# Performance work log

Hardware: AMD Instinct MI355X
Metric: run time of the kernel (lower is better)

Reference implementation:

```python
import jax, jax.numpy as jnp
import numpy as np

B, L = 128, 4096
H, RH, D, K = 128, 64, 64, 512  # num_hiddens, residual_hiddens, embedding_dim, num_embeddings
BETA = 0.25  # commitment_cost


def conv1d(x, w, b=None, stride=1, pad=0):
    # x: (N, C, W); w: (O, I, K) torch layout
    y = jax.lax.conv_general_dilated(x, w, (stride,), [(pad, pad)],
                                     dimension_numbers=('NCW', 'OIW', 'NCW'))
    return y if b is None else y + b[None, :, None]


def convT1d(x, w, b=None, stride=2, pad=1):
    # torch ConvTranspose1d weight layout (in, out, k)
    k = w.shape[-1]
    w_t = jnp.flip(w, -1).transpose(1, 0, 2)  # (out, in, k)
    y = jax.lax.conv_general_dilated(x, w_t, (1,), [(k - 1 - pad, k - 1 - pad)],
                                     lhs_dilation=(stride,),
                                     dimension_numbers=('NCW', 'OIW', 'NCW'))
    return y if b is None else y + b[None, :, None]


def res_stack(x, layers):
    for w1, w2 in layers:
        h = conv1d(jax.nn.relu(x), w1, None, 1, 1)
        h = conv1d(jax.nn.relu(h), w2, None, 1, 0)
        x = x + h
    return jax.nn.relu(x)


def _forward(x, enc_w1, enc_b1, enc_w2, enc_b2, enc_w3, enc_b3,
             enc_r1a, enc_r1b, enc_r2a, enc_r2b, pre_vq_w, pre_vq_b, codebook,
             dec_w1, dec_b1, dec_r1a, dec_r1b, dec_r2a, dec_r2b,
             dec_ct1_w, dec_ct1_b, dec_ct2_w, dec_ct2_b):
    # ---- Encoder (compression_factor == 4) ----
    h = x[:, None, :]                                   # (B, 1, L)
    h = jax.nn.relu(conv1d(h, enc_w1, enc_b1, 2, 1))    # (B, H/2, L/2)
    h = jax.nn.relu(conv1d(h, enc_w2, enc_b2, 2, 1))    # (B, H, L/4)
    h = conv1d(h, enc_w3, enc_b3, 1, 1)
    h = res_stack(h, [(enc_r1a, enc_r1b), (enc_r2a, enc_r2b)])
    z = conv1d(h, pre_vq_w, pre_vq_b, 1, 0)             # (B, D, T)

    # ---- Vector quantization ----
    zt = z.transpose(0, 2, 1)                           # (B, T, D)
    flat = zt.reshape(-1, D)                            # (BT, D)
    dists = (jnp.sum(flat * flat, 1, keepdims=True)
             - 2.0 * flat @ codebook.T
             + jnp.sum(codebook * codebook, 1))         # (BT, K)
    idx = jnp.argmin(dists, axis=1)                     # (BT,)
    q = codebook[idx].reshape(zt.shape)                 # (B, T, D)

    e_latent = jnp.mean((jax.lax.stop_gradient(q) - zt) ** 2)
    q_latent = jnp.mean((q - jax.lax.stop_gradient(zt)) ** 2)
    loss = q_latent + BETA * e_latent
    q_st = zt + jax.lax.stop_gradient(q - zt)           # straight-through

    counts = jnp.zeros((K,), flat.dtype).at[idx].add(1.0)
    probs = counts / idx.shape[0]
    perplexity = jnp.exp(-jnp.sum(probs * jnp.log(probs + 1e-10)))

    # ---- Decoder (compression_factor == 4) ----
    hd = q_st.transpose(0, 2, 1)                        # (B, D, T)
    hd = conv1d(hd, dec_w1, dec_b1, 1, 1)               # (B, H, T)
    hd = res_stack(hd, [(dec_r1a, dec_r1b), (dec_r2a, dec_r2b)])
    hd = jax.nn.relu(convT1d(hd, dec_ct1_w, dec_ct1_b)) # (B, H/2, 2T)
    hd = convT1d(hd, dec_ct2_w, dec_ct2_b)              # (B, 1, 4T)
    recon = jnp.squeeze(hd)                             # (B, L)
    return loss, recon, perplexity


def setup_inputs() -> dict:
    key = jax.random.key(0)
    ks = jax.random.split(key, 32)
    n = lambda i, shape, s=0.05: jax.random.normal(ks[i], shape, jnp.float32) * s
    inp = {
        'x': jax.random.normal(ks[0], (B, L), jnp.float32),
        'enc_w1': n(1, (H // 2, 1, 4)), 'enc_b1': jnp.zeros((H // 2,), jnp.float32),
        'enc_w2': n(2, (H, H // 2, 4)), 'enc_b2': jnp.zeros((H,), jnp.float32),
        'enc_w3': n(3, (H, H, 3)), 'enc_b3': jnp.zeros((H,), jnp.float32),
        'enc_r1a': n(4, (RH, H, 3)), 'enc_r1b': n(5, (H, RH, 1)),
        'enc_r2a': n(6, (RH, H, 3)), 'enc_r2b': n(7, (H, RH, 1)),
        'pre_vq_w': n(8, (D, H, 1)), 'pre_vq_b': jnp.zeros((D,), jnp.float32),
        'codebook': jax.random.uniform(ks[9], (K, D), jnp.float32, -1.0 / K, 1.0 / K),
        'dec_w1': n(10, (H, D, 3)), 'dec_b1': jnp.zeros((H,), jnp.float32),
        'dec_r1a': n(11, (RH, H, 3)), 'dec_r1b': n(12, (H, RH, 1)),
        'dec_r2a': n(13, (RH, H, 3)), 'dec_r2b': n(14, (H, RH, 1)),
        'dec_ct1_w': n(15, (H, H // 2, 4)), 'dec_ct1_b': jnp.zeros((H // 2,), jnp.float32),
        'dec_ct2_w': n(16, (H // 2, 1, 4)), 'dec_ct2_b': jnp.zeros((1,), jnp.float32),
    }
    return inp


def reference(x, enc_w1, enc_b1, enc_w2, enc_b2, enc_w3, enc_b3,
              enc_r1a, enc_r1b, enc_r2a, enc_r2b, pre_vq_w, pre_vq_b, codebook,
              dec_w1, dec_b1, dec_r1a, dec_r1b, dec_r2a, dec_r2b,
              dec_ct1_w, dec_ct1_b, dec_ct2_w, dec_ct2_b):
    return _forward(x, enc_w1, enc_b1, enc_w2, enc_b2, enc_w3, enc_b3,
                    enc_r1a, enc_r1b, enc_r2a, enc_r2b, pre_vq_w, pre_vq_b, codebook,
                    dec_w1, dec_b1, dec_r1a, dec_r1b, dec_r2a, dec_r2b,
                    dec_ct1_w, dec_ct1_b, dec_ct2_w, dec_ct2_b)
```

## Files before the change

kernel.cpp:

```cpp
#include <hip/hip_runtime.h>
#include <hip/hip_bf16.h>
#include <math.h>

using bf16 = __hip_bfloat16;
typedef __attribute__((ext_vector_type(4))) float f32x4;
typedef __attribute__((ext_vector_type(8))) short s16x8;

#define MFMA16(a,b,c) __builtin_amdgcn_mfma_f32_16x16x32_bf16((a),(b),(c),0,0,0)


__device__ inline float bf2f(unsigned short u) {
    union { float f; unsigned v; } c; c.v = ((unsigned)u) << 16; return c.f;
}
__device__ inline unsigned short bfbits(float f) {
    union { bf16 h; unsigned short u; } c; c.h = __float2bfloat16(f); return c.u;
}
__device__ inline s16x8 relu8(s16x8 v) {
#pragma unroll
    for (int j = 0; j < 8; ++j)
        v[j] = (short)(((unsigned short)v[j] & 0x8000u) ? 0 : (unsigned short)v[j]);
    return v;
}

__global__ __launch_bounds__(256, 3) void encmid_k(
    const bf16* __restrict__ in, const bf16* __restrict__ w3t,
    const float* __restrict__ b3, const bf16* __restrict__ r1w1,
    const bf16* __restrict__ r1w2, const bf16* __restrict__ r2w1,
    const bf16* __restrict__ r2w2, bf16* __restrict__ out)
{
    __shared__ __align__(16) char smem[47872];
    char* sY = smem;
    char* sX = smem + 21760;
    char* sH = smem + 21760;
    const int tid = threadIdx.x;
    const int b   = blockIdx.y;
    const int l0  = blockIdx.x * 64;
    const bf16* inb = in + (size_t)b * 1024 * 128;

    for (int i = tid; i < 96 * 16; i += 256) {
        int t = i >> 4, c0 = (i & 15) * 8;
        int g = l0 - 16 + t;
        s16x8 v = {};
        if (g >= 0 && g < 1024) v = *(const s16x8*)(inb + (size_t)g * 128 + c0);
        *(s16x8*)(sX + ((t * 136 + c0) << 1)) = v;
    }
    __syncthreads();

    const int lane = tid & 63;
    const int wid  = __builtin_amdgcn_readfirstlane(tid >> 6);
    const int lr   = lane & 15;
    const int kg   = lane >> 4;
    const f32x4 zf4 = {0.f, 0.f, 0.f, 0.f};

    {
        const int co0 = wid * 32;
        f32x4 acc[2][5];
#pragma unroll
        for (int cf = 0; cf < 2; ++cf)
#pragma unroll
            for (int lf = 0; lf < 5; ++lf) acc[cf][lf] = zf4;
#pragma unroll
        for (int k = 0; k < 3; ++k) {
            const bf16* Ab = w3t + (size_t)k * 128 * 128;
#pragma unroll
            for (int ks = 0; ks < 4; ++ks) {
                s16x8 af[2];
#pragma unroll
                for (int cf = 0; cf < 2; ++cf)
                    af[cf] = *(const s16x8*)(Ab + (co0 + cf * 16 + lr) * 128 + ks * 32 + kg * 8);
                s16x8 bfr[5];
#pragma unroll
                for (int lf = 0; lf < 5; ++lf) {
                    int tx = lf * 16 + lr + 7 + k;
                    bfr[lf] = *(const s16x8*)(sX + ((tx * 136 + ks * 32 + kg * 8) << 1));
                }
#pragma unroll
                for (int cf = 0; cf < 2; ++cf)
#pragma unroll
                    for (int lf = 0; lf < 5; ++lf)
                        acc[cf][lf] = MFMA16(af[cf], bfr[lf], acc[cf][lf]);
            }
        }
        __syncthreads();
#pragma unroll
        for (int cf = 0; cf < 2; ++cf)
#pragma unroll
            for (int lf = 0; lf < 5; ++lf) {
                int row = lf * 16 + lr;
                int p   = l0 - 8 + row;
                int cb0 = co0 + cf * 16 + kg * 4;
                bool ok = (p >= 0 && p < 1024);
                float r[4];
#pragma unroll
                for (int j = 0; j < 4; ++j)
                    r[j] = ok ? (acc[cf][lf][j] + b3[cb0 + j]) : 0.f;
                uint2 pk;
                pk.x = (unsigned)bfbits(r[0]) | ((unsigned)bfbits(r[1]) << 16);
                pk.y = (unsigned)bfbits(r[2]) | ((unsigned)bfbits(r[3]) << 16);
                *(uint2*)(sY + ((row * 136 + cb0) << 1)) = pk;
            }
    }
    __syncthreads();

#pragma unroll 1
    for (int blk = 0; blk < 2; ++blk) {
        const bf16* w1 = blk ? r2w1 : r1w1;
        {
            const int co0 = wid * 16;
            f32x4 acc[5];
#pragma unroll
            for (int lf = 0; lf < 5; ++lf) acc[lf] = zf4;
#pragma unroll
            for (int k = 0; k < 3; ++k) {
                const bf16* Ab = w1 + (size_t)k * 64 * 128;
#pragma unroll
                for (int ks = 0; ks < 4; ++ks) {
                    s16x8 a = *(const s16x8*)(Ab + (co0 + lr) * 128 + ks * 32 + kg * 8);
                    s16x8 bfr[5];
#pragma unroll
                    for (int lf = 0; lf < 5; ++lf) {
                        int ry = lf * 16 + lr + k - 1;
                        ry = (ry < 0) ? 0 : (ry > 79 ? 79 : ry);
                        bfr[lf] = relu8(*(const s16x8*)(sY + ((ry * 136 + ks * 32 + kg * 8) << 1)));
                    }
#pragma unroll
                    for (int lf = 0; lf < 5; ++lf)
                        acc[lf] = MFMA16(a, bfr[lf], acc[lf]);
                }
            }
#pragma unroll
            for (int lf = 0; lf < 5; ++lf) {
                int row = lf * 16 + lr;
                int ch0 = co0 + kg * 4;
                uint2 pk;
                pk.x = (unsigned)bfbits(fmaxf(acc[lf][0], 0.f)) |
                       ((unsigned)bfbits(fmaxf(acc[lf][1], 0.f)) << 16);
                pk.y = (unsigned)bfbits(fmaxf(acc[lf][2], 0.f)) |
                       ((unsigned)bfbits(fmaxf(acc[lf][3], 0.f)) << 16);
                *(uint2*)(sH + ((row * 72 + ch0) << 1)) = pk;
            }
        }
        __syncthreads();

        if (blk == 0) {
            const int co0 = wid * 32;
            f32x4 acc[2][5];
#pragma unroll
            for (int cf = 0; cf < 2; ++cf)
#pragma unroll
                for (int lf = 0; lf < 5; ++lf) acc[cf][lf] = zf4;
#pragma unroll
            for (int ks = 0; ks < 2; ++ks) {
                s16x8 af[2];
#pragma unroll
                for (int cf = 0; cf < 2; ++cf)
                    af[cf] = *(const s16x8*)(r1w2 + (size_t)(co0 + cf * 16 + lr) * 64 + ks * 32 + kg * 8);
                s16x8 bfr[5];
#pragma unroll
                for (int lf = 0; lf < 5; ++lf) {
                    int row = lf * 16 + lr;
                    bfr[lf] = *(const s16x8*)(sH + ((row * 72 + ks * 32 + kg * 8) << 1));
                }
#pragma unroll
                for (int cf = 0; cf < 2; ++cf)
#pragma unroll
                    for (int lf = 0; lf < 5; ++lf)
                        acc[cf][lf] = MFMA16(af[cf], bfr[lf], acc[cf][lf]);
            }
#pragma unroll
            for (int cf = 0; cf < 2; ++cf)
#pragma unroll
                for (int lf = 0; lf < 5; ++lf) {
                    int row = lf * 16 + lr;
                    int p   = l0 - 8 + row;
                    int cb0 = co0 + cf * 16 + kg * 4;
                    uint2 old = *(const uint2*)(sY + ((row * 136 + cb0) << 1));
                    bool ok = (p >= 0 && p < 1024);
                    float r[4];
                    r[0] = acc[cf][lf][0] + bf2f((unsigned short)(old.x & 0xffff));
                    r[1] = acc[cf][lf][1] + bf2f((unsigned short)(old.x >> 16));
                    r[2] = acc[cf][lf][2] + bf2f((unsigned short)(old.y & 0xffff));
                    r[3] = acc[cf][lf][3] + bf2f((unsigned short)(old.y >> 16));
                    uint2 pk;
                    pk.x = ok ? ((unsigned)bfbits(r[0]) | ((unsigned)bfbits(r[1]) << 16)) : 0u;
                    pk.y = ok ? ((unsigned)bfbits(r[2]) | ((unsigned)bfbits(r[3]) << 16)) : 0u;
                    *(uint2*)(sY + ((row * 136 + cb0) << 1)) = pk;
                }
            __syncthreads();
        } else {
            const int co0 = wid * 32;
            f32x4 acc[2][4];
#pragma unroll
            for (int cf = 0; cf < 2; ++cf)
#pragma unroll
                for (int lf = 0; lf < 4; ++lf) acc[cf][lf] = zf4;
#pragma unroll
            for (int ks = 0; ks < 2; ++ks) {
                s16x8 af[2];
#pragma unroll
                for (int cf = 0; cf < 2; ++cf)
                    af[cf] = *(const s16x8*)(r2w2 + (size_t)(co0 + cf * 16 + lr) * 64 + ks * 32 + kg * 8);
                s16x8 bfr[4];
#pragma unroll
                for (int lf = 0; lf < 4; ++lf) {
                    int row = 8 + lf * 16 + lr;
                    bfr[lf] = *(const s16x8*)(sH + ((row * 72 + ks * 32 + kg * 8) << 1));
                }
#pragma unroll
                for (int cf = 0; cf < 2; ++cf)
#pragma unroll
                    for (int lf = 0; lf < 4; ++lf)
                        acc[cf][lf] = MFMA16(af[cf], bfr[lf], acc[cf][lf]);
            }
#pragma unroll
            for (int cf = 0; cf < 2; ++cf)
#pragma unroll
                for (int lf = 0; lf < 4; ++lf) {
                    int row = 8 + lf * 16 + lr;
                    int cb0 = co0 + cf * 16 + kg * 4;
                    uint2 old = *(const uint2*)(sY + ((row * 136 + cb0) << 1));
                    float r[4];
                    r[0] = fmaxf(acc[cf][lf][0] + bf2f((unsigned short)(old.x & 0xffff)), 0.f);
                    r[1] = fmaxf(acc[cf][lf][1] + bf2f((unsigned short)(old.x >> 16)), 0.f);
                    r[2] = fmaxf(acc[cf][lf][2] + bf2f((unsigned short)(old.y & 0xffff)), 0.f);
                    r[3] = fmaxf(acc[cf][lf][3] + bf2f((unsigned short)(old.y >> 16)), 0.f);
                    uint2 pk;
                    pk.x = (unsigned)bfbits(r[0]) | ((unsigned)bfbits(r[1]) << 16);
                    pk.y = (unsigned)bfbits(r[2]) | ((unsigned)bfbits(r[3]) << 16);
                    *(uint2*)(out + ((size_t)b * 1024 + l0 + lf * 16 + lr) * 128 + cb0) = pk;
                }
        }
    }
}

__global__ __launch_bounds__(256, 4) void decmid_k(
    const bf16* __restrict__ qin, const bf16* __restrict__ dw1,
    const float* __restrict__ db1, const bf16* __restrict__ r1w1,
    const bf16* __restrict__ r1w2, const bf16* __restrict__ r2w1,
    const bf16* __restrict__ r2w2, const bf16* __restrict__ ct1w,
    const float* __restrict__ ct1b, bf16* __restrict__ out)
{
    __shared__ __align__(16) char smem[35584];
    char* sY = smem;
    char* sQ = smem + 21760;
    char* sH = smem + 21760;
    const int tid = threadIdx.x;
    const int b   = blockIdx.y;
    const int l0  = blockIdx.x * 64;
    const bf16* inb = qin + (size_t)b * 1024 * 64;

    for (int i = tid; i < 96 * 8; i += 256) {
        int t = i >> 3, c0 = (i & 7) * 8;
        int g = l0 - 16 + t;
        s16x8 v = {};
        if (g >= 0 && g < 1024) v = *(const s16x8*)(inb + (size_t)g * 64 + c0);
        *(s16x8*)(sQ + ((t * 72 + c0) << 1)) = v;
    }
    __syncthreads();

    const int lane = tid & 63;
    const int wid  = __builtin_amdgcn_readfirstlane(tid >> 6);
    const int lr   = lane & 15;
    const int kg   = lane >> 4;
    const f32x4 zf4 = {0.f, 0.f, 0.f, 0.f};

    {
        const int co0 = wid * 32;
        f32x4 acc[2][5];
#pragma unroll
        for (int cf = 0; cf < 2; ++cf)
#pragma unroll
            for (int lf = 0; lf < 5; ++lf) acc[cf][lf] = zf4;
#pragma unroll
        for (int k = 0; k < 3; ++k) {
            const bf16* Ab = dw1 + (size_t)k * 128 * 64;
#pragma unroll
            for (int ks = 0; ks < 2; ++ks) {
                s16x8 af[2];
#pragma unroll
                for (int cf = 0; cf < 2; ++cf)
                    af[cf] = *(const s16x8*)(Ab + (co0 + cf * 16 + lr) * 64 + ks * 32 + kg * 8);
                s16x8 bfr[5];
#pragma unroll
                for (int lf = 0; lf < 5; ++lf) {
                    int tx = lf * 16 + lr + 7 + k;
                    bfr[lf] = *(const s16x8*)(sQ + ((tx * 72 + ks * 32 + kg * 8) << 1));
                }
#pragma unroll
                for (int cf = 0; cf < 2; ++cf)
#pragma unroll
                    for (int lf = 0; lf < 5; ++lf)
                        acc[cf][lf] = MFMA16(af[cf], bfr[lf], acc[cf][lf]);
            }
        }
        __syncthreads();
#pragma unroll
        for (int cf = 0; cf < 2; ++cf)
#pragma unroll
            for (int lf = 0; lf < 5; ++lf) {
                int row = lf * 16 + lr;
                int p   = l0 - 8 + row;
                int cb0 = co0 + cf * 16 + kg * 4;
                bool ok = (p >= 0 && p < 1024);
                float r[4];
#pragma unroll
                for (int j = 0; j < 4; ++j)
                    r[j] = ok ? (acc[cf][lf][j] + db1[cb0 + j]) : 0.f;
                uint2 pk;
                pk.x = (unsigned)bfbits(r[0]) | ((unsigned)bfbits(r[1]) << 16);
                pk.y = (unsigned)bfbits(r[2]) | ((unsigned)bfbits(r[3]) << 16);
                *(uint2*)(sY + ((row * 136 + cb0) << 1)) = pk;
            }
    }
    __syncthreads();

#pragma unroll 1
    for (int blk = 0; blk < 2; ++blk) {
        const bf16* w1 = blk ? r2w1 : r1w1;
        const bf16* w2 = blk ? r2w2 : r1w2;
        {
            const int co0 = wid * 16;
            f32x4 acc[5];
#pragma unroll
            for (int lf = 0; lf < 5; ++lf) acc[lf] = zf4;
#pragma unroll
            for (int k = 0; k < 3; ++k) {
                const bf16* Ab = w1 + (size_t)k * 64 * 128;
#pragma unroll
                for (int ks = 0; ks < 4; ++ks) {
                    s16x8 a = *(const s16x8*)(Ab + (co0 + lr) * 128 + ks * 32 + kg * 8);
                    s16x8 bfr[5];
#pragma unroll
                    for (int lf = 0; lf < 5; ++lf) {
                        int ry = lf * 16 + lr + k - 1;
                        ry = (ry < 0) ? 0 : (ry > 79 ? 79 : ry);
                        bfr[lf] = relu8(*(const s16x8*)(sY + ((ry * 136 + ks * 32 + kg * 8) << 1)));
                    }
#pragma unroll
                    for (int lf = 0; lf < 5; ++lf)
                        acc[lf] = MFMA16(a, bfr[lf], acc[lf]);
                }
            }
#pragma unroll
            for (int lf = 0; lf < 5; ++lf) {
                int row = lf * 16 + lr;
                int ch0 = co0 + kg * 4;
                uint2 pk;
                pk.x = (unsigned)bfbits(fmaxf(acc[lf][0], 0.f)) |
                       ((unsigned)bfbits(fmaxf(acc[lf][1], 0.f)) << 16);
                pk.y = (unsigned)bfbits(fmaxf(acc[lf][2], 0.f)) |
                       ((unsigned)bfbits(fmaxf(acc[lf][3], 0.f)) << 16);
                *(uint2*)(sH + ((row * 72 + ch0) << 1)) = pk;
            }
        }
        __syncthreads();
        {
            const int co0 = wid * 32;
            f32x4 acc[2][5];
#pragma unroll
            for (int cf = 0; cf < 2; ++cf)
#pragma unroll
                for (int lf = 0; lf < 5; ++lf) acc[cf][lf] = zf4;
#pragma unroll
            for (int ks = 0; ks < 2; ++ks) {
                s16x8 af[2];
#pragma unroll
                for (int cf = 0; cf < 2; ++cf)
                    af[cf] = *(const s16x8*)(w2 + (size_t)(co0 + cf * 16 + lr) * 64 + ks * 32 + kg * 8);
                s16x8 bfr[5];
#pragma unroll
                for (int lf = 0; lf < 5; ++lf) {
                    int row = lf * 16 + lr;
                    bfr[lf] = *(const s16x8*)(sH + ((row * 72 + ks * 32 + kg * 8) << 1));
                }
#pragma unroll
                for (int cf = 0; cf < 2; ++cf)
#pragma unroll
                    for (int lf = 0; lf < 5; ++lf)
                        acc[cf][lf] = MFMA16(af[cf], bfr[lf], acc[cf][lf]);
            }
#pragma unroll
            for (int cf = 0; cf < 2; ++cf)
#pragma unroll
                for (int lf = 0; lf < 5; ++lf) {
                    int row = lf * 16 + lr;
                    int p   = l0 - 8 + row;
                    int cb0 = co0 + cf * 16 + kg * 4;
                    uint2 old = *(const uint2*)(sY + ((row * 136 + cb0) << 1));
                    bool ok = (p >= 0 && p < 1024);
                    float r[4];
                    r[0] = acc[cf][lf][0] + bf2f((unsigned short)(old.x & 0xffff));
                    r[1] = acc[cf][lf][1] + bf2f((unsigned short)(old.x >> 16));
                    r[2] = acc[cf][lf][2] + bf2f((unsigned short)(old.y & 0xffff));
                    r[3] = acc[cf][lf][3] + bf2f((unsigned short)(old.y >> 16));
                    if (blk == 1)
#pragma unroll
                        for (int j = 0; j < 4; ++j) r[j] = fmaxf(r[j], 0.f);
                    uint2 pk;
                    pk.x = ok ? ((unsigned)bfbits(r[0]) | ((unsigned)bfbits(r[1]) << 16)) : 0u;
                    pk.y = ok ? ((unsigned)bfbits(r[2]) | ((unsigned)bfbits(r[3]) << 16)) : 0u;
                    *(uint2*)(sY + ((row * 136 + cb0) << 1)) = pk;
                }
        }
        __syncthreads();
    }

    {
        const int co0 = (wid & 1) * 32;
        const int mh  = wid >> 1;
        f32x4 acc[2][2][2];
#pragma unroll
        for (int g = 0; g < 2; ++g)
#pragma unroll
            for (int cf = 0; cf < 2; ++cf)
#pragma unroll
                for (int j = 0; j < 2; ++j) acc[g][cf][j] = zf4;
#pragma unroll
        for (int g = 0; g < 2; ++g)
#pragma unroll
            for (int k = 0; k < 2; ++k) {
                const bf16* Ab = ct1w + (size_t)(g * 2 + k) * 64 * 128;
                const int doff = (g == 0) ? (k - 1) : k;
#pragma unroll
                for (int ks = 0; ks < 4; ++ks) {
                    s16x8 af[2];
#pragma unroll
                    for (int cf = 0; cf < 2; ++cf)
                        af[cf] = *(const s16x8*)(Ab + (co0 + cf * 16 + lr) * 128 + ks * 32 + kg * 8);
                    s16x8 bfr[2];
#pragma unroll
                    for (int j = 0; j < 2; ++j) {
                        int ty = 8 + (mh * 2 + j) * 16 + lr + doff;
                        bfr[j] = *(const s16x8*)(sY + ((ty * 136 + ks * 32 + kg * 8) << 1));
                    }
#pragma unroll
                    for (int cf = 0; cf < 2; ++cf)
#pragma unroll
                        for (int j = 0; j < 2; ++j)
                            acc[g][cf][j] = MFMA16(af[cf], bfr[j], acc[g][cf][j]);
                }
            }
#pragma unroll
        for (int g = 0; g < 2; ++g)
#pragma unroll
            for (int cf = 0; cf < 2; ++cf)
#pragma unroll
                for (int j = 0; j < 2; ++j) {
                    int m   = (mh * 2 + j) * 16 + lr;
                    int cb0 = co0 + cf * 16 + kg * 4;
                    float r[4];
#pragma unroll
                    for (int jj = 0; jj < 4; ++jj)
                        r[jj] = fmaxf(acc[g][cf][j][jj] + ct1b[cb0 + jj], 0.f);
                    uint2 pk;
                    pk.x = (unsigned)bfbits(r[0]) | ((unsigned)bfbits(r[1]) << 16);
                    pk.y = (unsigned)bfbits(r[2]) | ((unsigned)bfbits(r[3]) << 16);
                    *(uint2*)(out + ((size_t)b * 2048 + 2 * (l0 + m) + g) * 64 + cb0) = pk;
                }
    }
}

__global__ __launch_bounds__(256) void enc12_k(
    const float* __restrict__ x, const float* __restrict__ w1,
    const float* __restrict__ b1, const bf16* __restrict__ w2t,
    const float* __restrict__ b2, bf16* __restrict__ out)
{
    __shared__ float sXf[268];
    __shared__ float sW1[256];
    __shared__ float sB1[64];
    __shared__ __align__(16) char sX[132 * 144];
    const int tid = threadIdx.x;
    const int b   = blockIdx.y;
    const int l0  = blockIdx.x * 64;
    const float* xb = x + (size_t)b * 4096;

    for (int i = tid; i < 266; i += 256) {
        int g = 4 * l0 - 3 + i;
        sXf[i] = (g >= 0 && g < 4096) ? xb[g] : 0.f;
    }
    if (tid < 256) sW1[tid] = w1[tid];
    if (tid < 64)  sB1[tid] = b1[tid];
    __syncthreads();

    for (int i = tid; i < 132 * 64; i += 256) {
        int t = i >> 6, c = i & 63;
        int p = (t < 66) ? 2 * (l0 + t) : 2 * (l0 + t - 66) - 1;
        float v = 0.f;
        if (p >= 0 && p < 2048) {
            int xi = 2 * p - 4 * l0 + 2;
            float a = sB1[c];
#pragma unroll
            for (int k = 0; k < 4; ++k) a = fmaf(sXf[xi + k], sW1[c * 4 + k], a);
            v = fmaxf(a, 0.f);
        }
        *(bf16*)(sX + ((t * 72 + c) << 1)) = __float2bfloat16(v);
    }
    __syncthreads();

    const int lane = tid & 63;
    const int wid  = __builtin_amdgcn_readfirstlane(tid >> 6);
    const int co0  = wid * 32;
    const int lr   = lane & 15;
    const int kg   = lane >> 4;

    f32x4 acc[2][4];
#pragma unroll
    for (int cf = 0; cf < 2; ++cf)
#pragma unroll
        for (int lf = 0; lf < 4; ++lf) acc[cf][lf] = (f32x4){0.f, 0.f, 0.f, 0.f};

#pragma unroll
    for (int k = 0; k < 4; ++k) {
        const int roff = (k == 0) ? 66 : (k == 1) ? 0 : (k == 2) ? 67 : 1;
        const bf16* Ab = w2t + (size_t)k * 128 * 64;
#pragma unroll
        for (int ks = 0; ks < 2; ++ks) {
            s16x8 af[2];
#pragma unroll
            for (int cf = 0; cf < 2; ++cf)
                af[cf] = *(const s16x8*)(Ab + (co0 + cf * 16 + lr) * 64 + ks * 32 + kg * 8);
            s16x8 bfr[4];
#pragma unroll
            for (int lf = 0; lf < 4; ++lf) {
                int t = roff + lf * 16 + lr;
                bfr[lf] = *(const s16x8*)(sX + ((t * 72 + ks * 32 + kg * 8) << 1));
            }
#pragma unroll
            for (int cf = 0; cf < 2; ++cf)
#pragma unroll
                for (int lf = 0; lf < 4; ++lf)
                    acc[cf][lf] = MFMA16(af[cf], bfr[lf], acc[cf][lf]);
        }
    }

#pragma unroll
    for (int cf = 0; cf < 2; ++cf)
#pragma unroll
        for (int lf = 0; lf < 4; ++lf) {
            int cb0  = co0 + cf * 16 + kg * 4;
            int lcol = lf * 16 + lr;
            float r[4];
#pragma unroll
            for (int j = 0; j < 4; ++j)
                r[j] = fmaxf(acc[cf][lf][j] + b2[cb0 + j], 0.f);
            uint2 pk;
            pk.x = (unsigned)bfbits(r[0]) | ((unsigned)bfbits(r[1]) << 16);
            pk.y = (unsigned)bfbits(r[2]) | ((unsigned)bfbits(r[3]) << 16);
            *(uint2*)(out + ((size_t)b * 1024 + l0 + lcol) * 128 + cb0) = pk;
        }
}

__global__ __launch_bounds__(256) void ct2_k(
    const bf16* __restrict__ in, const float* __restrict__ w,
    const float* __restrict__ bias, float* __restrict__ out)
{
    __shared__ __align__(16) char sX[258 * 144];
    const int tid = threadIdx.x;
    const int b   = blockIdx.y;
    const int m0  = blockIdx.x * 256;
    const bf16* inb = in + (size_t)b * 2048 * 64;
    for (int i = tid; i < 258 * 8; i += 256) {
        int t = i >> 3, c0 = (i & 7) * 8;
        int g = m0 - 1 + t;
        s16x8 v = {};
        if (g >= 0 && g < 2048) v = *(const s16x8*)(inb + (size_t)g * 64 + c0);
        *(s16x8*)(sX + ((t * 72 + c0) << 1)) = v;
    }
    __syncthreads();
    float e = bias[0], o = bias[0];
#pragma unroll
    for (int c0 = 0; c0 < 64; c0 += 8) {
        s16x8 vm1 = *(const s16x8*)(sX + (((tid + 0) * 72 + c0) << 1));
        s16x8 v0  = *(const s16x8*)(sX + (((tid + 1) * 72 + c0) << 1));
        s16x8 vp1 = *(const s16x8*)(sX + (((tid + 2) * 72 + c0) << 1));
#pragma unroll
        for (int j = 0; j < 8; ++j) {
            int ci = c0 + j;
            float xm1 = bf2f((unsigned short)vm1[j]);
            float x0  = bf2f((unsigned short)v0[j]);
            float xp1 = bf2f((unsigned short)vp1[j]);
            e = fmaf(x0,  w[ci * 4 + 1], fmaf(xm1, w[ci * 4 + 3], e));
            o = fmaf(xp1, w[ci * 4 + 0], fmaf(x0,  w[ci * 4 + 2], o));
        }
    }
    int m = m0 + tid;
    out[(size_t)b * 4096 + 2 * m]     = e;
    out[(size_t)b * 4096 + 2 * m + 1] = o;
}

__global__ __launch_bounds__(256) void wx_k(
    const float* ew2, const float* ew3, const float* er1a, const float* er1b,
    const float* er2a, const float* er2b, const float* pvw, const float* dw1,
    const float* dr1a, const float* dr1b, const float* dr2a, const float* dr2b,
    const float* ct1w, bf16* wb)
{
    const int job = blockIdx.x;
    bf16* dst = wb + (size_t)job * 65536;
    const float* src; int CO, CI, K;
    switch (job) {
        case 0:  src = ew2;  CO = 128; CI = 64;  K = 4; break;
        case 1:  src = ew3;  CO = 128; CI = 128; K = 3; break;
        case 2:  src = er1a; CO = 64;  CI = 128; K = 3; break;
        case 3:  src = er1b; CO = 128; CI = 64;  K = 1; break;
        case 4:  src = er2a; CO = 64;  CI = 128; K = 3; break;
        case 5:  src = er2b; CO = 128; CI = 64;  K = 1; break;
        case 6:  src = pvw;  CO = 64;  CI = 128; K = 1; break;
        case 7:  src = dw1;  CO = 128; CI = 64;  K = 3; break;
        case 8:  src = dr1a; CO = 64;  CI = 128; K = 3; break;
        case 9:  src = dr1b; CO = 128; CI = 64;  K = 1; break;
        case 10: src = dr2a; CO = 64;  CI = 128; K = 3; break;
        case 11: src = dr2b; CO = 128; CI = 64;  K = 1; break;
        default: src = ct1w; CO = 64;  CI = 128; K = 4; break;
    }
    const int tot = CO * CI * K;
    for (int i = blockIdx.y * 256 + threadIdx.x; i < tot; i += gridDim.y * 256) {
        if (job < 12) {
            int k = i / (CO * CI); int r = i - k * CO * CI;
            int co = r / CI; int ci = r - co * CI;
            dst[i] = __float2bfloat16(src[((size_t)co * CI + ci) * K + k]);
        } else {
            const int TAP[4] = {3, 1, 2, 0};
            int g = i / (64 * 128); int r = i - g * 64 * 128;
            int co = r / 128; int ci = r - co * 128;
            dst[i] = __float2bfloat16(src[((size_t)ci * 64 + co) * 4 + TAP[g]]);
        }
    }
}

__global__ __launch_bounds__(256) void cbprep_k(
    const float* __restrict__ cb, bf16* __restrict__ cbh, bf16* __restrict__ cbl,
    float* __restrict__ sc)
{
    int k = blockIdx.x * 256 + threadIdx.x;
    const float* c = cb + (size_t)k * 64;
    float s = 0.f;
#pragma unroll
    for (int d = 0; d < 64; ++d) s = fmaf(c[d], c[d], s);
    sc[k] = s;
#pragma unroll
    for (int c0 = 0; c0 < 64; c0 += 8) {
        union { unsigned short u[8]; s16x8 v; } ph, pl;
#pragma unroll
        for (int j = 0; j < 8; ++j) {
            float v = c[c0 + j];
            unsigned short h = bfbits(v);
            ph.u[j] = h;
            pl.u[j] = bfbits(v - bf2f(h));
        }
        *(s16x8*)(cbh + (size_t)k * 64 + c0) = ph.v;
        *(s16x8*)(cbl + (size_t)k * 64 + c0) = pl.v;
    }
}

__global__ __launch_bounds__(256, 4) void vqf_k(
    const bf16* __restrict__ A, const bf16* __restrict__ pvw,
    const float* __restrict__ pvb, const float* __restrict__ cbf,
    const bf16* __restrict__ cbh, const bf16* __restrict__ cbl,
    const float* __restrict__ sc, bf16* __restrict__ q,
    float* __restrict__ counts, float* __restrict__ loss_sum)
{
    __shared__ __align__(16) char sMem[34816];
    __shared__ float sSC[512];
    __shared__ float sHist[512];
    __shared__ int   sBK[128];
    __shared__ float sWS[4];
    const int tid = threadIdx.x;
    sSC[tid] = sc[tid]; sSC[tid + 256] = sc[tid + 256];
    sHist[tid] = 0.f;   sHist[tid + 256] = 0.f;

    const int n0 = blockIdx.x * 128;
    for (int i = tid; i < 128 * 16; i += 256) {
        int t = i >> 4, c0 = (i & 15) * 8;
        s16x8 v = *(const s16x8*)(A + (size_t)(n0 + t) * 128 + c0);
        *(s16x8*)(sMem + ((t * 136 + c0) << 1)) = v;
    }
    __syncthreads();

    const int lane = tid & 63, wid = tid >> 6;
    const int lr = lane & 15, kg = lane >> 4;
    const int pw0 = wid * 32;
    const f32x4 zf4 = {0.f, 0.f, 0.f, 0.f};

    f32x4 zacc[4][2];
#pragma unroll
    for (int cf = 0; cf < 4; ++cf)
#pragma unroll
        for (int lf = 0; lf < 2; ++lf) zacc[cf][lf] = zf4;
#pragma unroll
    for (int ks = 0; ks < 4; ++ks) {
        s16x8 af[4];
#pragma unroll
        for (int cf = 0; cf < 4; ++cf)
            af[cf] = *(const s16x8*)(pvw + (size_t)(cf * 16 + lr) * 128 + ks * 32 + kg * 8);
        s16x8 bfr[2];
#pragma unroll
        for (int lf = 0; lf < 2; ++lf) {
            int t = pw0 + lf * 16 + lr;
            bfr[lf] = *(const s16x8*)(sMem + ((t * 136 + ks * 32 + kg * 8) << 1));
        }
#pragma unroll
        for (int cf = 0; cf < 4; ++cf)
// ... 199 lines not shown
```

Before: 357.6 us.

## Retile encoder/decoder MFMA work as 2x2 channel-row wave grid and stage ct1 output

```diff
diff --git a/kernel.cpp b/kernel.cpp
--- a/kernel.cpp
+++ b/kernel.cpp
@@ -20,6 +20,12 @@
     for (int j = 0; j < 8; ++j)
         v[j] = (short)(((unsigned short)v[j] & 0x8000u) ? 0 : (unsigned short)v[j]);
     return v;
+}
+__device__ inline uint2 pack4(float a, float b, float c, float d) {
+    uint2 p;
+    p.x = (unsigned)bfbits(a) | ((unsigned)bfbits(b) << 16);
+    p.y = (unsigned)bfbits(c) | ((unsigned)bfbits(d) << 16);
+    return p;
 }
 
 __global__ __launch_bounds__(256, 3) void encmid_k(
@@ -50,185 +56,200 @@
     const int wid  = __builtin_amdgcn_readfirstlane(tid >> 6);
     const int lr   = lane & 15;
     const int kg   = lane >> 4;
+    const int ci   = wid & 1;
+    const int rj   = wid >> 1;
+    const int nrf  = rj ? 2 : 3;
+    const int rf0  = rj ? 3 : 0;
     const f32x4 zf4 = {0.f, 0.f, 0.f, 0.f};
 
     {
-        const int co0 = wid * 32;
-        f32x4 acc[2][5];
-#pragma unroll
-        for (int cf = 0; cf < 2; ++cf)
-#pragma unroll
-            for (int lf = 0; lf < 5; ++lf) acc[cf][lf] = zf4;
+        f32x4 acc[4][3];
+#pragma unroll
+        for (int cf = 0; cf < 4; ++cf)
+#pragma unroll
+            for (int rr = 0; rr < 3; ++rr) acc[cf][rr] = zf4;
 #pragma unroll
         for (int k = 0; k < 3; ++k) {
             const bf16* Ab = w3t + (size_t)k * 128 * 128;
 #pragma unroll
             for (int ks = 0; ks < 4; ++ks) {
-                s16x8 af[2];
-#pragma unroll
-                for (int cf = 0; cf < 2; ++cf)
-                    af[cf] = *(const s16x8*)(Ab + (co0 + cf * 16 + lr) * 128 + ks * 32 + kg * 8);
-                s16x8 bfr[5];
-#pragma unroll
-                for (int lf = 0; lf < 5; ++lf) {
-                    int tx = lf * 16 + lr + 7 + k;
-                    bfr[lf] = *(const s16x8*)(sX + ((tx * 136 + ks * 32 + kg * 8) << 1));
-                }
-#pragma unroll
-                for (int cf = 0; cf < 2; ++cf)
-#pragma unroll
-                    for (int lf = 0; lf < 5; ++lf)
-                        acc[cf][lf] = MFMA16(af[cf], bfr[lf], acc[cf][lf]);
-            }
-        }
-        __syncthreads();
-#pragma unroll
-        for (int cf = 0; cf < 2; ++cf)
-#pragma unroll
-            for (int lf = 0; lf < 5; ++lf) {
-                int row = lf * 16 + lr;
+                const int cc = ks * 32 + kg * 8;
+                s16x8 af[4];
+#pragma unroll
+                for (int cf = 0; cf < 4; ++cf)
+                    af[cf] = *(const s16x8*)(Ab + (ci * 64 + cf * 16 + lr) * 128 + cc);
+                s16x8 bfr[3];
+#pragma unroll
+                for (int rr = 0; rr < 3; ++rr)
+                    if (rr < nrf) {
+                        int tx = (rf0 + rr) * 16 + lr + 7 + k;
+                        bfr[rr] = *(const s16x8*)(sX + ((tx * 136 + cc) << 1));
+                    }
+#pragma unroll
+                for (int cf = 0; cf < 4; ++cf)
+#pragma unroll
+                    for (int rr = 0; rr < 3; ++rr)
+                        if (rr < nrf)
+                            acc[cf][rr] = MFMA16(af[cf], bfr[rr], acc[cf][rr]);
+            }
+        }
+#pragma unroll
+        for (int rr = 0; rr < 3; ++rr)
+            if (rr < nrf) {
+                int row = (rf0 + rr) * 16 + lr;
                 int p   = l0 - 8 + row;
-                int cb0 = co0 + cf * 16 + kg * 4;
                 bool ok = (p >= 0 && p < 1024);
-                float r[4];
-#pragma unroll
-                for (int j = 0; j < 4; ++j)
-                    r[j] = ok ? (acc[cf][lf][j] + b3[cb0 + j]) : 0.f;
-                uint2 pk;
-                pk.x = (unsigned)bfbits(r[0]) | ((unsigned)bfbits(r[1]) << 16);
-                pk.y = (unsigned)bfbits(r[2]) | ((unsigned)bfbits(r[3]) << 16);
-                *(uint2*)(sY + ((row * 136 + cb0) << 1)) = pk;
+#pragma unroll
+                for (int cf = 0; cf < 4; ++cf) {
+                    int ch0 = ci * 64 + cf * 16 + kg * 4;
+                    float r[4];
+#pragma unroll
+                    for (int j = 0; j < 4; ++j)
+                        r[j] = ok ? (acc[cf][rr][j] + b3[ch0 + j]) : 0.f;
+                    *(uint2*)(sY + ((row * 136 + ch0) << 1)) = pack4(r[0], r[1], r[2], r[3]);
+                }
             }
     }
     __syncthreads();
 
 #pragma unroll 1
-    for (int blk = 0; blk < 2; ++blk) {
-        const bf16* w1 = blk ? r2w1 : r1w1;
+    for (int blk2 = 0; blk2 < 2; ++blk2) {
+        const bf16* w1 = blk2 ? r2w1 : r1w1;
+        const bf16* w2 = blk2 ? r2w2 : r1w2;
         {
-            const int co0 = wid * 16;
-            f32x4 acc[5];
-#pragma unroll
-            for (int lf = 0; lf < 5; ++lf) acc[lf] = zf4;
+            f32x4 acc[2][3];
+#pragma unroll
+            for (int cf = 0; cf < 2; ++cf)
+#pragma unroll
+                for (int rr = 0; rr < 3; ++rr) acc[cf][rr] = zf4;
 #pragma unroll
             for (int k = 0; k < 3; ++k) {
                 const bf16* Ab = w1 + (size_t)k * 64 * 128;
 #pragma unroll
                 for (int ks = 0; ks < 4; ++ks) {
-                    s16x8 a = *(const s16x8*)(Ab + (co0 + lr) * 128 + ks * 32 + kg * 8);
-                    s16x8 bfr[5];
-#pragma unroll
-                    for (int lf = 0; lf < 5; ++lf) {
-                        int ry = lf * 16 + lr + k - 1;
-                        ry = (ry < 0) ? 0 : (ry > 79 ? 79 : ry);
-                        bfr[lf] = relu8(*(const s16x8*)(sY + ((ry * 136 + ks * 32 + kg * 8) << 1)));
+                    const int cc = ks * 32 + kg * 8;
+                    s16x8 af[2];
+#pragma unroll
+                    for (int cf = 0; cf < 2; ++cf)
+                        af[cf] = *(const s16x8*)(Ab + (ci * 32 + cf * 16 + lr) * 128 + cc);
+                    s16x8 bfr[3];
+#pragma unroll
+                    for (int rr = 0; rr < 3; ++rr)
+                        if (rr < nrf) {
+                            int ry = (rf0 + rr) * 16 + lr + k - 1;
+                            ry = (ry < 0) ? 0 : (ry > 79 ? 79 : ry);
+                            bfr[rr] = relu8(*(const s16x8*)(sY + ((ry * 136 + cc) << 1)));
+                        }
+#pragma unroll
+                    for (int cf = 0; cf < 2; ++cf)
+#pragma unroll
+                        for (int rr = 0; rr < 3; ++rr)
+                            if (rr < nrf)
+                                acc[cf][rr] = MFMA16(af[cf], bfr[rr], acc[cf][rr]);
+                }
+            }
+#pragma unroll
+            for (int rr = 0; rr < 3; ++rr)
+                if (rr < nrf) {
+                    int row = (rf0 + rr) * 16 + lr;
+#pragma unroll
+                    for (int cf = 0; cf < 2; ++cf) {
+                        int ch0 = ci * 32 + cf * 16 + kg * 4;
+                        *(uint2*)(sH + ((row * 72 + ch0) << 1)) =
+                            pack4(fmaxf(acc[cf][rr][0], 0.f), fmaxf(acc[cf][rr][1], 0.f),
+                                  fmaxf(acc[cf][rr][2], 0.f), fmaxf(acc[cf][rr][3], 0.f));
                     }
-#pragma unroll
-                    for (int lf = 0; lf < 5; ++lf)
-                        acc[lf] = MFMA16(a, bfr[lf], acc[lf]);
-                }
-            }
-#pragma unroll
-            for (int lf = 0; lf < 5; ++lf) {
-                int row = lf * 16 + lr;
-                int ch0 = co0 + kg * 4;
-                uint2 pk;
-                pk.x = (unsigned)bfbits(fmaxf(acc[lf][0], 0.f)) |
-                       ((unsigned)bfbits(fmaxf(acc[lf][1], 0.f)) << 16);
-                pk.y = (unsigned)bfbits(fmaxf(acc[lf][2], 0.f)) |
-                       ((unsigned)bfbits(fmaxf(acc[lf][3], 0.f)) << 16);
-                *(uint2*)(sH + ((row * 72 + ch0) << 1)) = pk;
-            }
+                }
         }
         __syncthreads();
 
-        if (blk == 0) {
-            const int co0 = wid * 32;
-            f32x4 acc[2][5];
-#pragma unroll
-            for (int cf = 0; cf < 2; ++cf)
-#pragma unroll
-                for (int lf = 0; lf < 5; ++lf) acc[cf][lf] = zf4;
+        if (blk2 == 0) {
+            f32x4 acc[4][3];
+#pragma unroll
+            for (int cf = 0; cf < 4; ++cf)
+#pragma unroll
+                for (int rr = 0; rr < 3; ++rr) acc[cf][rr] = zf4;
 #pragma unroll
             for (int ks = 0; ks < 2; ++ks) {
-                s16x8 af[2];
-#pragma unroll
-                for (int cf = 0; cf < 2; ++cf)
-                    af[cf] = *(const s16x8*)(r1w2 + (size_t)(co0 + cf * 16 + lr) * 64 + ks * 32 + kg * 8);
-                s16x8 bfr[5];
-#pragma unroll
-                for (int lf = 0; lf < 5; ++lf) {
-                    int row = lf * 16 + lr;
-                    bfr[lf] = *(const s16x8*)(sH + ((row * 72 + ks * 32 + kg * 8) << 1));
-                }
-#pragma unroll
-                for (int cf = 0; cf < 2; ++cf)
-#pragma unroll
-                    for (int lf = 0; lf < 5; ++lf)
-                        acc[cf][lf] = MFMA16(af[cf], bfr[lf], acc[cf][lf]);
-            }
-#pragma unroll
-            for (int cf = 0; cf < 2; ++cf)
-#pragma unroll
-                for (int lf = 0; lf < 5; ++lf) {
-                    int row = lf * 16 + lr;
-                    int p   = l0 - 8 + row;
-                    int cb0 = co0 + cf * 16 + kg * 4;
-                    uint2 old = *(const uint2*)(sY + ((row * 136 + cb0) << 1));
-                    bool ok = (p >= 0 && p < 1024);
-                    float r[4];
-                    r[0] = acc[cf][lf][0] + bf2f((unsigned short)(old.x & 0xffff));
-                    r[1] = acc[cf][lf][1] + bf2f((unsigned short)(old.x >> 16));
-                    r[2] = acc[cf][lf][2] + bf2f((unsigned short)(old.y & 0xffff));
-                    r[3] = acc[cf][lf][3] + bf2f((unsigned short)(old.y >> 16));
-                    uint2 pk;
-                    pk.x = ok ? ((unsigned)bfbits(r[0]) | ((unsigned)bfbits(r[1]) << 16)) : 0u;
-                    pk.y = ok ? ((unsigned)bfbits(r[2]) | ((unsigned)bfbits(r[3]) << 16)) : 0u;
-                    *(uint2*)(sY + ((row * 136 + cb0) << 1)) = pk;
+                const int cc = ks * 32 + kg * 8;
+                s16x8 af[4];
+#pragma unroll
+                for (int cf = 0; cf < 4; ++cf)
+                    af[cf] = *(const s16x8*)(w2 + (size_t)(ci * 64 + cf * 16 + lr) * 64 + cc);
+                s16x8 bfr[3];
+#pragma unroll
+                for (int rr = 0; rr < 3; ++rr)
+                    if (rr < nrf) {
+                        int row = (rf0 + rr) * 16 + lr;
+                        bfr[rr] = *(const s16x8*)(sH + ((row * 72 + cc) << 1));
+                    }
+#pragma unroll
+                for (int cf = 0; cf < 4; ++cf)
+#pragma unroll
+                    for (int rr = 0; rr < 3; ++rr)
+                        if (rr < nrf)
+                            acc[cf][rr] = MFMA16(af[cf], bfr[rr], acc[cf][rr]);
+            }
+#pragma unroll
+            for (int rr = 0; rr < 3; ++rr)
+                if (rr < nrf) {
+                    int row = (rf0 + rr) * 16 + lr;
+                    bool ok = (l0 - 8 + row >= 0 && l0 - 8 + row < 1024);
+#pragma unroll
+                    for (int cf = 0; cf < 4; ++cf) {
+                        int ch0 = ci * 64 + cf * 16 + kg * 4;
+                        uint2 old = *(const uint2*)(sY + ((row * 136 + ch0) << 1));
+                        float r0 = acc[cf][rr][0] + bf2f((unsigned short)(old.x & 0xffff));
+                        float r1 = acc[cf][rr][1] + bf2f((unsigned short)(old.x >> 16));
+                        float r2 = acc[cf][rr][2] + bf2f((unsigned short)(old.y & 0xffff));
+                        float r3 = acc[cf][rr][3] + bf2f((unsigned short)(old.y >> 16));
+                        uint2 pk = pack4(r0, r1, r2, r3);
+                        if (!ok) { pk.x = 0u; pk.y = 0u; }
+                        *(uint2*)(sY + ((row * 136 + ch0) << 1)) = pk;
+                    }
                 }
             __syncthreads();
         } else {
-            const int co0 = wid * 32;
-            f32x4 acc[2][4];
-#pragma unroll
-            for (int cf = 0; cf < 2; ++cf)
-#pragma unroll
-                for (int lf = 0; lf < 4; ++lf) acc[cf][lf] = zf4;
+            f32x4 acc[4][2];
+#pragma unroll
+            for (int cf = 0; cf < 4; ++cf)
+#pragma unroll
+                for (int rr = 0; rr < 2; ++rr) acc[cf][rr] = zf4;
 #pragma unroll
             for (int ks = 0; ks < 2; ++ks) {
-                s16x8 af[2];
-#pragma unroll
-                for (int cf = 0; cf < 2; ++cf)
-                    af[cf] = *(const s16x8*)(r2w2 + (size_t)(co0 + cf * 16 + lr) * 64 + ks * 32 + kg * 8);
-                s16x8 bfr[4];
-#pragma unroll
-                for (int lf = 0; lf < 4; ++lf) {
-                    int row = 8 + lf * 16 + lr;
-                    bfr[lf] = *(const s16x8*)(sH + ((row * 72 + ks * 32 + kg * 8) << 1));
-                }
-#pragma unroll
-                for (int cf = 0; cf < 2; ++cf)
-#pragma unroll
-                    for (int lf = 0; lf < 4; ++lf)
-                        acc[cf][lf] = MFMA16(af[cf], bfr[lf], acc[cf][lf]);
-            }
-#pragma unroll
-            for (int cf = 0; cf < 2; ++cf)
-#pragma unroll
-                for (int lf = 0; lf < 4; ++lf) {
-                    int row = 8 + lf * 16 + lr;
-                    int cb0 = co0 + cf * 16 + kg * 4;
-                    uint2 old = *(const uint2*)(sY + ((row * 136 + cb0) << 1));
-                    float r[4];
-                    r[0] = fmaxf(acc[cf][lf][0] + bf2f((unsigned short)(old.x & 0xffff)), 0.f);
-                    r[1] = fmaxf(acc[cf][lf][1] + bf2f((unsigned short)(old.x >> 16)), 0.f);
-                    r[2] = fmaxf(acc[cf][lf][2] + bf2f((unsigned short)(old.y & 0xffff)), 0.f);
-                    r[3] = fmaxf(acc[cf][lf][3] + bf2f((unsigned short)(old.y >> 16)), 0.f);
-                    uint2 pk;
-                    pk.x = (unsigned)bfbits(r[0]) | ((unsigned)bfbits(r[1]) << 16);
-                    pk.y = (unsigned)bfbits(r[2]) | ((unsigned)bfbits(r[3]) << 16);
-                    *(uint2*)(out + ((size_t)b * 1024 + l0 + lf * 16 + lr) * 128 + cb0) = pk;
-                }
+                const int cc = ks * 32 + kg * 8;
+                s16x8 af[4];
+#pragma unroll
+                for (int cf = 0; cf < 4; ++cf)
+                    af[cf] = *(const s16x8*)(w2 + (size_t)(ci * 64 + cf * 16 + lr) * 64 + cc);
+                s16x8 bfr[2];
+#pragma unroll
+                for (int rr = 0; rr < 2; ++rr) {
+                    int row = 8 + (2 * rj + rr) * 16 + lr;
+                    bfr[rr] = *(const s16x8*)(sH + ((row * 72 + cc) << 1));
+                }
+#pragma unroll
+                for (int cf = 0; cf < 4; ++cf)
+#pragma unroll
+                    for (int rr = 0; rr < 2; ++rr)
+                        acc[cf][rr] = MFMA16(af[cf], bfr[rr], acc[cf][rr]);
+            }
+#pragma unroll
+            for (int rr = 0; rr < 2; ++rr) {
+                int lf  = 2 * rj + rr;
+                int row = 8 + lf * 16 + lr;
+#pragma unroll
+                for (int cf = 0; cf < 4; ++cf) {
+                    int ch0 = ci * 64 + cf * 16 + kg * 4;
+                    uint2 old = *(const uint2*)(sY + ((row * 136 + ch0) << 1));
+                    float r0 = fmaxf(acc[cf][rr][0] + bf2f((unsigned short)(old.x & 0xffff)), 0.f);
+                    float r1 = fmaxf(acc[cf][rr][1] + bf2f((unsigned short)(old.x >> 16)), 0.f);
+                    float r2 = fmaxf(acc[cf][rr][2] + bf2f((unsigned short)(old.y & 0xffff)), 0.f);
+                    float r3 = fmaxf(acc[cf][rr][3] + bf2f((unsigned short)(old.y >> 16)), 0.f);
+                    *(uint2*)(out + ((size_t)b * 1024 + l0 + lf * 16 + lr) * 128 + ch0) =
+                        pack4(r0, r1, r2, r3);
+                }
+            }
         }
     }
 }
@@ -262,144 +283,161 @@
     const int wid  = __builtin_amdgcn_readfirstlane(tid >> 6);
     const int lr   = lane & 15;
     const int kg   = lane >> 4;
+    const int ci   = wid & 1;
+    const int rj   = wid >> 1;
+    const int nrf  = rj ? 2 : 3;
+    const int rf0  = rj ? 3 : 0;
     const f32x4 zf4 = {0.f, 0.f, 0.f, 0.f};
 
     {
-        const int co0 = wid * 32;
-        f32x4 acc[2][5];
-#pragma unroll
-        for (int cf = 0; cf < 2; ++cf)
-#pragma unroll
-            for (int lf = 0; lf < 5; ++lf) acc[cf][lf] = zf4;
+        f32x4 acc[4][3];
+#pragma unroll
+        for (int cf = 0; cf < 4; ++cf)
+#pragma unroll
+            for (int rr = 0; rr < 3; ++rr) acc[cf][rr] = zf4;
 #pragma unroll
         for (int k = 0; k < 3; ++k) {
             const bf16* Ab = dw1 + (size_t)k * 128 * 64;
 #pragma unroll
             for (int ks = 0; ks < 2; ++ks) {
-                s16x8 af[2];
-#pragma unroll
-                for (int cf = 0; cf < 2; ++cf)
-                    af[cf] = *(const s16x8*)(Ab + (co0 + cf * 16 + lr) * 64 + ks * 32 + kg * 8);
-                s16x8 bfr[5];
-#pragma unroll
-                for (int lf = 0; lf < 5; ++lf) {
-                    int tx = lf * 16 + lr + 7 + k;
-                    bfr[lf] = *(const s16x8*)(sQ + ((tx * 72 + ks * 32 + kg * 8) << 1));
-                }
-#pragma unroll
-                for (int cf = 0; cf < 2; ++cf)
-#pragma unroll
-                    for (int lf = 0; lf < 5; ++lf)
-                        acc[cf][lf] = MFMA16(af[cf], bfr[lf], acc[cf][lf]);
+                const int cc = ks * 32 + kg * 8;
+                s16x8 af[4];
+#pragma unroll
+                for (int cf = 0; cf < 4; ++cf)
+                    af[cf] = *(const s16x8*)(Ab + (ci * 64 + cf * 16 + lr) * 64 + cc);
+                s16x8 bfr[3];
+#pragma unroll
+                for (int rr = 0; rr < 3; ++rr)
+                    if (rr < nrf) {
+                        int tx = (rf0 + rr) * 16 + lr + 7 + k;
+                        bfr[rr] = *(const s16x8*)(sQ + ((tx * 72 + cc) << 1));
+                    }
+#pragma unroll
+                for (int cf = 0; cf < 4; ++cf)
+#pragma unroll
+                    for (int rr = 0; rr < 3; ++rr)
+                        if (rr < nrf)
+                            acc[cf][rr] = MFMA16(af[cf], bfr[rr], acc[cf][rr]);
             }
         }
         __syncthreads();
 #pragma unroll
-        for (int cf = 0; cf < 2; ++cf)
-#pragma unroll
-            for (int lf = 0; lf < 5; ++lf) {
-                int row = lf * 16 + lr;
+        for (int rr = 0; rr < 3; ++rr)
+            if (rr < nrf) {
+                int row = (rf0 + rr) * 16 + lr;
                 int p   = l0 - 8 + row;
-                int cb0 = co0 + cf * 16 + kg * 4;
                 bool ok = (p >= 0 && p < 1024);
-                float r[4];
-#pragma unroll
-                for (int j = 0; j < 4; ++j)
-                    r[j] = ok ? (acc[cf][lf][j] + db1[cb0 + j]) : 0.f;
-                uint2 pk;
-                pk.x = (unsigned)bfbits(r[0]) | ((unsigned)bfbits(r[1]) << 16);
-                pk.y = (unsigned)bfbits(r[2]) | ((unsigned)bfbits(r[3]) << 16);
-                *(uint2*)(sY + ((row * 136 + cb0) << 1)) = pk;
+#pragma unroll
+                for (int cf = 0; cf < 4; ++cf) {
+                    int ch0 = ci * 64 + cf * 16 + kg * 4;
+                    float r[4];
+#pragma unroll
+                    for (int j = 0; j < 4; ++j)
+                        r[j] = ok ? (acc[cf][rr][j] + db1[ch0 + j]) : 0.f;
+                    *(uint2*)(sY + ((row * 136 + ch0) << 1)) = pack4(r[0], r[1], r[2], r[3]);
+                }
             }
     }
     __syncthreads();
 
 #pragma unroll 1
-    for (int blk = 0; blk < 2; ++blk) {
-        const bf16* w1 = blk ? r2w1 : r1w1;
-        const bf16* w2 = blk ? r2w2 : r1w2;
+    for (int blk2 = 0; blk2 < 2; ++blk2) {
+        const bf16* w1 = blk2 ? r2w1 : r1w1;
+        const bf16* w2 = blk2 ? r2w2 : r1w2;
         {
-            const int co0 = wid * 16;
-            f32x4 acc[5];
-#pragma unroll
-            for (int lf = 0; lf < 5; ++lf) acc[lf] = zf4;
+            f32x4 acc[2][3];
+#pragma unroll
+            for (int cf = 0; cf < 2; ++cf)
+#pragma unroll
+                for (int rr = 0; rr < 3; ++rr) acc[cf][rr] = zf4;
 #pragma unroll
             for (int k = 0; k < 3; ++k) {
                 const bf16* Ab = w1 + (size_t)k * 64 * 128;
 #pragma unroll
                 for (int ks = 0; ks < 4; ++ks) {
-                    s16x8 a = *(const s16x8*)(Ab + (co0 + lr) * 128 + ks * 32 + kg * 8);
-                    s16x8 bfr[5];
-#pragma unroll
-                    for (int lf = 0; lf < 5; ++lf) {
-                        int ry = lf * 16 + lr + k - 1;
-                        ry = (ry < 0) ? 0 : (ry > 79 ? 79 : ry);
-                        bfr[lf] = relu8(*(const s16x8*)(sY + ((ry * 136 + ks * 32 + kg * 8) << 1)));
+                    const int cc = ks * 32 + kg * 8;
+                    s16x8 af[2];
+#pragma unroll
+                    for (int cf = 0; cf < 2; ++cf)
+                        af[cf] = *(const s16x8*)(Ab + (ci * 32 + cf * 16 + lr) * 128 + cc);
+                    s16x8 bfr[3];
+#pragma unroll
+                    for (int rr = 0; rr < 3; ++rr)
+                        if (rr < nrf) {
+                            int ry = (rf0 + rr) * 16 + lr + k - 1;
+                            ry = (ry < 0) ? 0 : (ry > 79 ? 79 : ry);
+                            bfr[rr] = relu8(*(const s16x8*)(sY + ((ry * 136 + cc) << 1)));
+                        }
+#pragma unroll
+                    for (int cf = 0; cf < 2; ++cf)
+#pragma unroll
+                        for (int rr = 0; rr < 3; ++rr)
+                            if (rr < nrf)
+                                acc[cf][rr] = MFMA16(af[cf], bfr[rr], acc[cf][rr]);
+                }
+            }
+#pragma unroll
+            for (int rr = 0; rr < 3; ++rr)
+                if (rr < nrf) {
+                    int row = (rf0 + rr) * 16 + lr;
+#pragma unroll
+                    for (int cf = 0; cf < 2; ++cf) {
+                        int ch0 = ci * 32 + cf * 16 + kg * 4;
+                        *(uint2*)(sH + ((row * 72 + ch0) << 1)) =
+                            pack4(fmaxf(acc[cf][rr][0], 0.f), fmaxf(acc[cf][rr][1], 0.f),
+                                  fmaxf(acc[cf][rr][2], 0.f), fmaxf(acc[cf][rr][3], 0.f));
                     }
-#pragma unroll
-                    for (int lf = 0; lf < 5; ++lf)
-                        acc[lf] = MFMA16(a, bfr[lf], acc[lf]);
-                }
-            }
-#pragma unroll
-            for (int lf = 0; lf < 5; ++lf) {
-                int row = lf * 16 + lr;
-                int ch0 = co0 + kg * 4;
-                uint2 pk;
-                pk.x = (unsigned)bfbits(fmaxf(acc[lf][0], 0.f)) |
-                       ((unsigned)bfbits(fmaxf(acc[lf][1], 0.f)) << 16);
-                pk.y = (unsigned)bfbits(fmaxf(acc[lf][2], 0.f)) |
-                       ((unsigned)bfbits(fmaxf(acc[lf][3], 0.f)) << 16);
-                *(uint2*)(sH + ((row * 72 + ch0) << 1)) = pk;
-            }
+                }
         }
         __syncthreads();
         {
-            const int co0 = wid * 32;
-            f32x4 acc[2][5];
-#pragma unroll
-            for (int cf = 0; cf < 2; ++cf)
-#pragma unroll
-                for (int lf = 0; lf < 5; ++lf) acc[cf][lf] = zf4;
+            f32x4 acc[4][3];
+#pragma unroll
+            for (int cf = 0; cf < 4; ++cf)
+#pragma unroll
+                for (int rr = 0; rr < 3; ++rr) acc[cf][rr] = zf4;
 #pragma unroll
             for (int ks = 0; ks < 2; ++ks) {
-                s16x8 af[2];
-#pragma unroll
-                for (int cf = 0; cf < 2; ++cf)
-                    af[cf] = *(const s16x8*)(w2 + (size_t)(co0 + cf * 16 + lr) * 64 + ks * 32 + kg * 8);
-                s16x8 bfr[5];
-#pragma unroll
-                for (int lf = 0; lf < 5; ++lf) {
-                    int row = lf * 16 + lr;
-                    bfr[lf] = *(const s16x8*)(sH + ((row * 72 + ks * 32 + kg * 8) << 1));
-                }
-#pragma unroll
-                for (int cf = 0; cf < 2; ++cf)
-#pragma unroll
-                    for (int lf = 0; lf < 5; ++lf)
-                        acc[cf][lf] = MFMA16(af[cf], bfr[lf], acc[cf][lf]);
-            }
-#pragma unroll
-            for (int cf = 0; cf < 2; ++cf)
-#pragma unroll
-                for (int lf = 0; lf < 5; ++lf) {
-                    int row = lf * 16 + lr;
-                    int p   = l0 - 8 + row;
-                    int cb0 = co0 + cf * 16 + kg * 4;
-                    uint2 old = *(const uint2*)(sY + ((row * 136 + cb0) << 1));
-                    bool ok = (p >= 0 && p < 1024);
-                    float r[4];
-                    r[0] = acc[cf][lf][0] + bf2f((unsigned short)(old.x & 0xffff));
-                    r[1] = acc[cf][lf][1] + bf2f((unsigned short)(old.x >> 16));
-                    r[2] = acc[cf][lf][2] + bf2f((unsigned short)(old.y & 0xffff));
-                    r[3] = acc[cf][lf][3] + bf2f((unsigned short)(old.y >> 16));
-                    if (blk == 1)
-#pragma unroll
-                        for (int j = 0; j < 4; ++j) r[j] = fmaxf(r[j], 0.f);
-                    uint2 pk;
-                    pk.x = ok ? ((unsigned)bfbits(r[0]) | ((unsigned)bfbits(r[1]) << 16)) : 0u;
-                    pk.y = ok ? ((unsigned)bfbits(r[2]) | ((unsigned)bfbits(r[3]) << 16)) : 0u;
-                    *(uint2*)(sY + ((row * 136 + cb0) << 1)) = pk;
+                const int cc = ks * 32 + kg * 8;
+                s16x8 af[4];
+#pragma unroll
+                for (int cf = 0; cf < 4; ++cf)
+                    af[cf] = *(const s16x8*)(w2 + (size_t)(ci * 64 + cf * 16 + lr) * 64 + cc);
+                s16x8 bfr[3];
+#pragma unroll
+                for (int rr = 0; rr < 3; ++rr)
+                    if (rr < nrf) {
+                        int row = (rf0 + rr) * 16 + lr;
+                        bfr[rr] = *(const s16x8*)(sH + ((row * 72 + cc) << 1));
+                    }
+#pragma unroll
+                for (int cf = 0; cf < 4; ++cf)
+#pragma unroll
+                    for (int rr = 0; rr < 3; ++rr)
+                        if (rr < nrf)
+                            acc[cf][rr] = MFMA16(af[cf], bfr[rr], acc[cf][rr]);
+            }
+#pragma unroll
+            for (int rr = 0; rr < 3; ++rr)
+                if (rr < nrf) {
+                    int row = (rf0 + rr) * 16 + lr;
+                    bool ok = (l0 - 8 + row >= 0 && l0 - 8 + row < 1024);
+#pragma unroll
+                    for (int cf = 0; cf < 4; ++cf) {
+                        int ch0 = ci * 64 + cf * 16 + kg * 4;
+                        uint2 old = *(const uint2*)(sY + ((row * 136 + ch0) << 1));
+                        float r0 = acc[cf][rr][0] + bf2f((unsigned short)(old.x & 0xffff));
+                        float r1 = acc[cf][rr][1] + bf2f((unsigned short)(old.x >> 16));
+                        float r2 = acc[cf][rr][2] + bf2f((unsigned short)(old.y & 0xffff));
+                        float r3 = acc[cf][rr][3] + bf2f((unsigned short)(old.y >> 16));
+                        if (blk2 == 1) {
+                            r0 = fmaxf(r0, 0.f); r1 = fmaxf(r1, 0.f);
+                            r2 = fmaxf(r2, 0.f); r3 = fmaxf(r3, 0.f);
+                        }
+                        uint2 pk = pack4(r0, r1, r2, r3);
+                        if (!ok) { pk.x = 0u; pk.y = 0u; }
+                        *(uint2*)(sY + ((row * 136 + ch0) << 1)) = pk;
+                    }
                 }
         }
         __syncthreads();
@@ -423,15 +461,16 @@
                 const int doff = (g == 0) ? (k - 1) : k;
 #pragma unroll
                 for (int ks = 0; ks < 4; ++ks) {
+                    const int cc = ks * 32 + kg * 8;
                     s16x8 af[2];
 #pragma unroll
                     for (int cf = 0; cf < 2; ++cf)
-                        af[cf] = *(const s16x8*)(Ab + (co0 + cf * 16 + lr) * 128 + ks * 32 + kg * 8);
+                        af[cf] = *(const s16x8*)(Ab + (co0 + cf * 16 + lr) * 128 + cc);
                     s16x8 bfr[2];
 #pragma unroll
                     for (int j = 0; j < 2; ++j) {
                         int ty = 8 + (mh * 2 + j) * 16 + lr + doff;
-                        bfr[j] = *(const s16x8*)(sY + ((ty * 136 + ks * 32 + kg * 8) << 1));
+                        bfr[j] = *(const s16x8*)(sY + ((ty * 136 + cc) << 1));
                     }
 #pragma unroll
                     for (int cf = 0; cf < 2; ++cf)
@@ -440,6 +479,8 @@
                             acc[g][cf][j] = MFMA16(af[cf], bfr[j], acc[g][cf][j]);
                 }
             }
+        __syncthreads();
+
 #pragma unroll
         for (int g = 0; g < 2; ++g)
 #pragma unroll
@@ -447,16 +488,19 @@
 #pragma unroll
                 for (int j = 0; j < 2; ++j) {
                     int m   = (mh * 2 + j) * 16 + lr;
-                    int cb0 = co0 + cf * 16 + kg * 4;
+                    int rr  = 2 * m + g;
+                    int ch0 = co0 + cf * 16 + kg * 4;
                     float r[4];
 #pragma unroll
                     for (int jj = 0; jj < 4; ++jj)
-                        r[jj] = fmaxf(acc[g][cf][j][jj] + ct1b[cb0 + jj], 0.f);
-                    uint2 pk;
-                    pk.x = (unsigned)bfbits(r[0]) | ((unsigned)bfbits(r[1]) << 16);
-                    pk.y = (unsigned)bfbits(r[2]) | ((unsigned)bfbits(r[3]) << 16);
-                    *(uint2*)(out + ((size_t)b * 2048 + 2 * (l0 + m) + g) * 64 + cb0) = pk;
-                }
+                        r[jj] = fmaxf(acc[g][cf][j][jj] + ct1b[ch0 + jj], 0.f);
+                    *(uint2*)(sY + rr * 128 + ch0 * 2) = pack4(r[0], r[1], r[2], r[3]);
+                }
+        __syncthreads();
+
+        bf16* ob = out + ((size_t)b * 2048 + 2 * l0) * 64;
+        for (int i = tid; i < 1024; i += 256)
+            *(s16x8*)(ob + i * 8) = *(const s16x8*)(sY + i * 16);
     }
 }
 
@@ -543,10 +587,8 @@
 #pragma unroll
             for (int j = 0; j < 4; ++j)
                 r[j] = fmaxf(acc[cf][lf][j] + b2[cb0 + j], 0.f);
-            uint2 pk;
-            pk.x = (unsigned)bfbits(r[0]) | ((unsigned)bfbits(r[1]) << 16);
-            pk.y = (unsigned)bfbits(r[2]) | ((unsigned)bfbits(r[3]) << 16);
-            *(uint2*)(out + ((size_t)b * 1024 + l0 + lcol) * 128 + cb0) = pk;
+            *(uint2*)(out + ((size_t)b * 1024 + l0 + lcol) * 128 + cb0) =
+                pack4(r[0], r[1], r[2], r[3]);
         }
 }
 
```

Result: slower. 450.9 us (+26.1%).
